# Performance work log

Hardware: AMD Instinct MI355X
Metric: run time of the kernel (lower is better)

Reference implementation:

```python
import jax, jax.numpy as jnp
import numpy as np

B, N, D, NNZ = 8, 8192, 64, 2097152

def setup_inputs() -> dict:
    key = jax.random.key(0)
    k1, k2, k3, k4, k5, k6, k7 = jax.random.split(key, 7)
    return {
        "A_batch": jax.random.randint(k1, (NNZ,), 0, B),
        "A_row": jax.random.randint(k2, (NNZ,), 0, N),
        "A_col": jax.random.randint(k3, (NNZ,), 0, N),
        "A_vals": jax.random.normal(k4, (NNZ,), dtype=jnp.float32),
        "X": jax.random.normal(k5, (B, N, D), dtype=jnp.float32),
        "X_mask": jax.random.randint(k6, (B, N), 0, 2).astype(bool),
        "tarX_mask": jax.random.randint(k7, (B, N), 0, 2).astype(bool),
    }

def reference(A_batch, A_row, A_col, A_vals, X, X_mask, tarX_mask):
    # spmamm(A, 2, X, 1, tarX.mask, 'sum'):
    # out[b,i,:] = sum_j A[b,i,j] * X_filled[b,j,:], masked by tarX_mask.
    X_filled = jnp.where(X_mask[..., None], X, 0.0)          # (B,N,D) masked fill
    msg = A_vals[:, None] * X_filled[A_batch, A_col]          # (NNZ,D) gather + scale
    seg = A_batch * N + A_row                                 # linearized (b,i) target
    out = jax.ops.segment_sum(msg, seg, num_segments=B * N).reshape(B, N, D)
    return jnp.where(tarX_mask[..., None], out, 0.0)
```

## Files before the change

### kernel.cpp

```cpp
#include <hip/hip_runtime.h>

#define NB 8
#define NN 8192
#define ND 64

#define NBKT 512
#define ROWS_PER_BKT 128
#define SUB 16
#define NSLOT (NBKT * SUB)
#define SUBCAP 128
#define BKT_CAP (SUB * SUBCAP)
#define CNT_STRIDE 16
#define SPILLCAP 16384

__device__ __forceinline__ bool detect_bytes_block(const void* xm_raw,
                                                   int* s_flag) {
    if (threadIdx.x == 0) *s_flag = 0;
    __syncthreads();
    const unsigned int* w = (const unsigned int*)xm_raw;
    if (threadIdx.x < 256 && w[threadIdx.x] > 1u) atomicOr(s_flag, 1);
    __syncthreads();
    return *s_flag != 0;
}

__device__ __forceinline__ unsigned int mask_at(const void* m, bool bytes, int i) {
    return bytes ? (unsigned int)((const unsigned char*)m)[i]
                 : ((const unsigned int*)m)[i];
}

__global__ void bin_kernel(const int* __restrict__ Ab, const int* __restrict__ Ar,
                           const int* __restrict__ Ac, const float* __restrict__ Av,
                           const void* __restrict__ Xm_raw,
                           const void* __restrict__ Tm_raw,
                           unsigned int* __restrict__ cnt,
                           int2* __restrict__ buckets,
                           unsigned int* __restrict__ spill_cnt,
                           int2* __restrict__ spill,
                           int nq) {
    __shared__ int s_flag;
    const bool bytes = detect_bytes_block(Xm_raw, &s_flag);

    const int sub = blockIdx.x & (SUB - 1);
    const int4*   Ab4 = (const int4*)Ab;
    const int4*   Ar4 = (const int4*)Ar;
    const int4*   Ac4 = (const int4*)Ac;
    const float4* Av4 = (const float4*)Av;
    int i = blockIdx.x * blockDim.x + threadIdx.x;
    const int str = gridDim.x * blockDim.x;
    for (; i < nq; i += str) {
        const int4   b4 = Ab4[i];
        const int4   r4 = Ar4[i];
        const int4   c4 = Ac4[i];
        const float4 v4 = Av4[i];
        const int   bs[4] = {b4.x, b4.y, b4.z, b4.w};
        const int   rs[4] = {r4.x, r4.y, r4.z, r4.w};
        const int   cs[4] = {c4.x, c4.y, c4.z, c4.w};
        const float vs[4] = {v4.x, v4.y, v4.z, v4.w};
        #pragma unroll
        for (int j = 0; j < 4; ++j) {
            const int seg  = bs[j] * NN + rs[j];
            const int xrow = bs[j] * NN + cs[j];
            if (mask_at(Tm_raw, bytes, seg) && mask_at(Xm_raw, bytes, xrow)) {
                const int slot = (seg >> 7) * SUB + sub;
                const unsigned int pos = atomicAdd(&cnt[slot * CNT_STRIDE], 1u);
                if (pos < SUBCAP) {
                    buckets[(size_t)slot * SUBCAP + pos] =
                        make_int2(xrow | ((seg & (ROWS_PER_BKT - 1)) << 16),
                                  __float_as_int(vs[j]));
                } else {
                    const unsigned int sp = atomicAdd(spill_cnt, 1u);
                    if (sp < SPILLCAP)
                        spill[sp] = make_int2(xrow | (seg << 16), __float_as_int(vs[j]));
                }
            }
        }
    }
}

__global__ __launch_bounds__(1024) void accum_kernel(const unsigned int* __restrict__ cnt,
                                                     const int2* __restrict__ buckets,
                                                     const float* __restrict__ X,
                                                     const unsigned int* __restrict__ spill_cnt,
                                                     const int2* __restrict__ spill,
                                                     float* __restrict__ out) {
    __shared__ int2 sorted[BKT_CAP];
    __shared__ unsigned int hist[ROWS_PER_BKT];
    __shared__ unsigned int rowstart[ROWS_PER_BKT + 1];
    __shared__ unsigned int cursor[ROWS_PER_BKT];
    __shared__ unsigned int s_n[SUB];
    __shared__ unsigned int s_nsp;

    const int bkt = blockIdx.x;
    const int t = threadIdx.x;

    if (t < ROWS_PER_BKT) hist[t] = 0;
    if (t < SUB) s_n[t] = min(cnt[(bkt * SUB + t) * CNT_STRIDE], (unsigned int)SUBCAP);
    if (t == 0) s_nsp = min(*spill_cnt, (unsigned int)SPILLCAP);
    __syncthreads();

    int2 e0s, e1s;
    int r0 = -1, r1 = -1;
    {
        int idx = t, sub = idx >> 7, off = idx & (SUBCAP - 1);
        if ((unsigned int)off < s_n[sub]) {
            e0s = buckets[(size_t)(bkt * SUB + sub) * SUBCAP + off];
            r0 = (e0s.x >> 16) & (ROWS_PER_BKT - 1);
            atomicAdd(&hist[r0], 1u);
        }
        idx = t + 1024; sub = idx >> 7; off = idx & (SUBCAP - 1);
        if ((unsigned int)off < s_n[sub]) {
            e1s = buckets[(size_t)(bkt * SUB + sub) * SUBCAP + off];
            r1 = (e1s.x >> 16) & (ROWS_PER_BKT - 1);
            atomicAdd(&hist[r1], 1u);
        }
    }
    __syncthreads();

    if (t < 64) {
        const unsigned int h0 = hist[t], h1 = hist[64 + t];
        unsigned int a = h0, b = h1;
        for (int off = 1; off < 64; off <<= 1) {
            unsigned int v = __shfl_up(a, off);
            if (t >= off) a += v;
        }
        const unsigned int atot = __shfl(a, 63);
        for (int off = 1; off < 64; off <<= 1) {
            unsigned int v = __shfl_up(b, off);
            if (t >= off) b += v;
        }
        rowstart[t]      = a - h0;
        rowstart[64 + t] = atot + b - h1;
        cursor[t]        = a - h0;
        cursor[64 + t]   = atot + b - h1;
        if (t == 63) rowstart[128] = atot + b;
    }
    __syncthreads();

    if (r0 >= 0) { const unsigned int p = atomicAdd(&cursor[r0], 1u); sorted[p] = e0s; }
    if (r1 >= 0) { const unsigned int p = atomicAdd(&cursor[r1], 1u); sorted[p] = e1s; }
    __syncthreads();

    const int wave = t >> 6;
    const int lane = t & 63;
    const int rbase = wave * 8;
    float acc[8];
    #pragma unroll
    for (int j = 0; j < 8; ++j) {
        unsigned int k = rowstart[rbase + j];
        const unsigned int ke = rowstart[rbase + j + 1];
        float a = 0.f;
        for (; k + 4 <= ke; k += 4) {
            const int2 e0 = sorted[k],     e1 = sorted[k + 1];
            const int2 e2 = sorted[k + 2], e3 = sorted[k + 3];
            const float x0 = X[((size_t)(e0.x & 0xFFFF) << 6) + lane];
            const float x1 = X[((size_t)(e1.x & 0xFFFF) << 6) + lane];
            const float x2 = X[((size_t)(e2.x & 0xFFFF) << 6) + lane];
            const float x3 = X[((size_t)(e3.x & 0xFFFF) << 6) + lane];
            a = fmaf(__int_as_float(e0.y), x0, a);
            a = fmaf(__int_as_float(e1.y), x1, a);
            a = fmaf(__int_as_float(e2.y), x2, a);
            a = fmaf(__int_as_float(e3.y), x3, a);
        }
        for (; k < ke; ++k) {
            const int2 e = sorted[k];
            a = fmaf(__int_as_float(e.y), X[((size_t)(e.x & 0xFFFF) << 6) + lane], a);
        }
        acc[j] = a;
    }

    if (s_nsp) {
        const int seglo = bkt * ROWS_PER_BKT;
        for (unsigned int k = 0; k < s_nsp; ++k) {
            const int2 e = spill[k];
            const int r = ((e.x >> 16) & 0xFFFF) - seglo;
            if (r >= rbase && r < rbase + 8) {
                const float xv = X[((size_t)(e.x & 0xFFFF) << 6) + lane];
                const float vv = __int_as_float(e.y);
                #pragma unroll
                for (int j = 0; j < 8; ++j)
                    if (r == rbase + j) acc[j] = fmaf(vv, xv, acc[j]);
            }
        }
    }

    float* obase = out + ((size_t)bkt * ROWS_PER_BKT + rbase) * ND + lane;
    #pragma unroll
    for (int j = 0; j < 8; ++j) obase[(size_t)j * ND] = acc[j];
}

__global__ void coo_scatter_kernel(const int* __restrict__ Ab,
                                   const int* __restrict__ Ar,
                                   const int* __restrict__ Ac,
                                   const float* __restrict__ Av,
                                   const float* __restrict__ X,
                                   const void* __restrict__ Xm_raw,
                                   const void* __restrict__ Tm_raw,
                                   float* __restrict__ out, int nnz) {
    __shared__ int s_flag;
    const bool bytes = detect_bytes_block(Xm_raw, &s_flag);
    const int groups_per_block = blockDim.x >> 6;
    const int g0 = blockIdx.x * groups_per_block + (threadIdx.x >> 6);
    const int gstr = gridDim.x * groups_per_block;
    const int lane = threadIdx.x & 63;
    for (int e = g0; e < nnz; e += gstr) {
        const int b = Ab[e];
        const int r = Ar[e];
        if (!mask_at(Tm_raw, bytes, b * NN + r)) continue;
        const int c = Ac[e];
        if (!mask_at(Xm_raw, bytes, b * NN + c)) continue;
        const float v = Av[e];
        const float x = X[((size_t)(b * NN + c)) * ND + lane];
        atomicAdd(&out[((size_t)(b * NN + r)) * ND + lane], v * x);
    }
}

extern "C" void kernel_launch(void* const* d_in, const int* in_sizes, int n_in,
                              void* d_out, int out_size, void* d_ws, size_t ws_size,
                              hipStream_t stream) {
    const int*   Ab = (const int*)d_in[0];
    const int*   Ar = (const int*)d_in[1];
    const int*   Ac = (const int*)d_in[2];
    const float* Av = (const float*)d_in[3];
    const float* X  = (const float*)d_in[4];
    const void*  Xm_raw = d_in[5];
    const void*  Tm_raw = d_in[6];
    float* out = (float*)d_out;

    const int nnz   = in_sizes[0];
    const int nmask = in_sizes[5];

    unsigned char* w = (unsigned char*)d_ws;
    unsigned int* cnt       = (unsigned int*)w;  w += (size_t)NSLOT * CNT_STRIDE * 4;
    unsigned int* spill_cnt = (unsigned int*)w;  w += 16;
    int2*         buckets   = (int2*)w;          w += (size_t)NSLOT * SUBCAP * 8;
    int2*         spill     = (int2*)w;          w += (size_t)SPILLCAP * 8;
    const size_t needed = (size_t)(w - (unsigned char*)d_ws);

    if (ws_size < needed || nmask != NBKT * ROWS_PER_BKT || (nnz & 3) || nnz > (1 << 22)) {
        hipMemsetAsync(d_out, 0, (size_t)out_size * sizeof(float), stream);
        coo_scatter_kernel<<<16384, 256, 0, stream>>>(Ab, Ar, Ac, Av, X,
                                                      Xm_raw, Tm_raw, out, nnz);
        return;
    }

    hipMemsetAsync(cnt, 0, (size_t)NSLOT * CNT_STRIDE * 4 + 16, stream);

    const int nq = nnz >> 2;
    bin_kernel<<<2048, 256, 0, stream>>>(Ab, Ar, Ac, Av, Xm_raw, Tm_raw,
                                         cnt, buckets, spill_cnt, spill, nq);
    accum_kernel<<<NBKT, 1024, 0, stream>>>(cnt, buckets, X, spill_cnt, spill, out);
}
```

Measured before the change: 149.9 us.

## Pack masks into bitsets in a prep kernel that also zeroes counters

Adds a small prep kernel that uses ballot to pack the X and target masks into 32-bit bitsets (8 KB each), and zeroes the bucket counters in place of the memset. The binning kernel then looks up mask bits from these compact bitsets, which fit in cache, instead of reading the raw byte or int masks with a per-block format check. The four mask lookups per vector are issued before any atomics so the loads can overlap. This costs an extra kernel launch, but the memset launch it replaces offsets that.

```diff
diff --git a/kernel.cpp b/kernel.cpp
--- a/kernel.cpp
+++ b/kernel.cpp
@@ -12,6 +12,8 @@
 #define BKT_CAP (SUB * SUBCAP)
 #define CNT_STRIDE 16
 #define SPILLCAP 16384
+#define NMASK (NB * NN)
+#define NWORDS (NMASK / 32)
 
 __device__ __forceinline__ bool detect_bytes_block(const void* xm_raw,
                                                    int* s_flag) {
@@ -28,18 +30,53 @@
                  : ((const unsigned int*)m)[i];
 }
 
+__global__ void prep_kernel(const void* __restrict__ xm_raw,
+                            const void* __restrict__ tm_raw,
+                            unsigned int* __restrict__ xbits,
+                            unsigned int* __restrict__ tbits,
+                            unsigned int* __restrict__ cnt,
+                            unsigned int* __restrict__ spill_cnt) {
+    __shared__ int s_flag;
+    const bool bytes = detect_bytes_block(xm_raw, &s_flag);
+    const int t = threadIdx.x;
+    const int lane = t & 63;
+
+    {
+        const int gt = blockIdx.x * 256 + t;
+        uint4* c4 = (uint4*)cnt;
+        #pragma unroll
+        for (int i = 0; i < 4; ++i)
+            c4[gt + i * 8192] = make_uint4(0u, 0u, 0u, 0u);
+        if (gt == 0) *spill_cnt = 0u;
+    }
+
+    const int base = blockIdx.x * 2048;
+    for (int off = 0; off < 2048; off += 256) {
+        const int idx = base + off + t;
+        const unsigned int xv = mask_at(xm_raw, bytes, idx);
+        const unsigned int tv = mask_at(tm_raw, bytes, idx);
+        const unsigned long long xb = __ballot(xv != 0u);
+        const unsigned long long tb = __ballot(tv != 0u);
+        if ((lane & 31) == 0) {
+            const unsigned int xw = (lane == 0) ? (unsigned int)xb
+                                                : (unsigned int)(xb >> 32);
+            const unsigned int tw = (lane == 0) ? (unsigned int)tb
+                                                : (unsigned int)(tb >> 32);
+            xbits[idx >> 5] = xw;
+            tbits[idx >> 5] = tw;
+        }
+    }
+}
+
 __global__ void bin_kernel(const int* __restrict__ Ab, const int* __restrict__ Ar,
                            const int* __restrict__ Ac, const float* __restrict__ Av,
-                           const void* __restrict__ Xm_raw,
-                           const void* __restrict__ Tm_raw,
+                           const unsigned int* __restrict__ xbits,
+                           const unsigned int* __restrict__ tbits,
                            unsigned int* __restrict__ cnt,
                            int2* __restrict__ buckets,
                            unsigned int* __restrict__ spill_cnt,
                            int2* __restrict__ spill,
                            int nq) {
-    __shared__ int s_flag;
-    const bool bytes = detect_bytes_block(Xm_raw, &s_flag);
-
     const int sub = blockIdx.x & (SUB - 1);
     const int4*   Ab4 = (const int4*)Ab;
     const int4*   Ar4 = (const int4*)Ar;
@@ -56,21 +93,31 @@
         const int   rs[4] = {r4.x, r4.y, r4.z, r4.w};
         const int   cs[4] = {c4.x, c4.y, c4.z, c4.w};
         const float vs[4] = {v4.x, v4.y, v4.z, v4.w};
+
+        int seg[4], xrow[4];
+        unsigned int ok[4];
         #pragma unroll
         for (int j = 0; j < 4; ++j) {
-            const int seg  = bs[j] * NN + rs[j];
-            const int xrow = bs[j] * NN + cs[j];
-            if (mask_at(Tm_raw, bytes, seg) && mask_at(Xm_raw, bytes, xrow)) {
-                const int slot = (seg >> 7) * SUB + sub;
+            seg[j]  = bs[j] * NN + rs[j];
+            xrow[j] = bs[j] * NN + cs[j];
+            const unsigned int tw = tbits[seg[j] >> 5];
+            const unsigned int xw = xbits[xrow[j] >> 5];
+            ok[j] = ((tw >> (seg[j] & 31)) & 1u) & ((xw >> (xrow[j] & 31)) & 1u);
+        }
+        #pragma unroll
+        for (int j = 0; j < 4; ++j) {
+            if (ok[j]) {
+                const int slot = (seg[j] >> 7) * SUB + sub;
                 const unsigned int pos = atomicAdd(&cnt[slot * CNT_STRIDE], 1u);
                 if (pos < SUBCAP) {
                     buckets[(size_t)slot * SUBCAP + pos] =
-                        make_int2(xrow | ((seg & (ROWS_PER_BKT - 1)) << 16),
+                        make_int2(xrow[j] | ((seg[j] & (ROWS_PER_BKT - 1)) << 16),
                                   __float_as_int(vs[j]));
                 } else {
                     const unsigned int sp = atomicAdd(spill_cnt, 1u);
                     if (sp < SPILLCAP)
-                        spill[sp] = make_int2(xrow | (seg << 16), __float_as_int(vs[j]));
+                        spill[sp] = make_int2(xrow[j] | (seg[j] << 16),
+                                              __float_as_int(vs[j]));
                 }
             }
         }
@@ -232,21 +279,23 @@
     unsigned char* w = (unsigned char*)d_ws;
     unsigned int* cnt       = (unsigned int*)w;  w += (size_t)NSLOT * CNT_STRIDE * 4;
     unsigned int* spill_cnt = (unsigned int*)w;  w += 16;
+    unsigned int* xbits     = (unsigned int*)w;  w += (size_t)NWORDS * 4;
+    unsigned int* tbits     = (unsigned int*)w;  w += (size_t)NWORDS * 4;
     int2*         buckets   = (int2*)w;          w += (size_t)NSLOT * SUBCAP * 8;
     int2*         spill     = (int2*)w;          w += (size_t)SPILLCAP * 8;
     const size_t needed = (size_t)(w - (unsigned char*)d_ws);
 
-    if (ws_size < needed || nmask != NBKT * ROWS_PER_BKT || (nnz & 3) || nnz > (1 << 22)) {
+    if (ws_size < needed || nmask != NMASK || (nnz & 3) || nnz > (1 << 22)) {
         hipMemsetAsync(d_out, 0, (size_t)out_size * sizeof(float), stream);
         coo_scatter_kernel<<<16384, 256, 0, stream>>>(Ab, Ar, Ac, Av, X,
                                                       Xm_raw, Tm_raw, out, nnz);
         return;
     }
 
-    hipMemsetAsync(cnt, 0, (size_t)NSLOT * CNT_STRIDE * 4 + 16, stream);
-
+    prep_kernel<<<32, 256, 0, stream>>>(Xm_raw, Tm_raw, xbits, tbits,
+                                        cnt, spill_cnt);
     const int nq = nnz >> 2;
-    bin_kernel<<<2048, 256, 0, stream>>>(Ab, Ar, Ac, Av, Xm_raw, Tm_raw,
+    bin_kernel<<<2048, 256, 0, stream>>>(Ab, Ar, Ac, Av, xbits, tbits,
                                          cnt, buckets, spill_cnt, spill, nq);
     accum_kernel<<<NBKT, 1024, 0, stream>>>(cnt, buckets, X, spill_cnt, spill, out);
 }
```

Measured after the change: 149.6 us. Within noise of the previous version (-0.2%).
